# Kernel tuning notes

Hardware: AMD Instinct MI355X
Metric: run time of the kernel (lower is better)

## Reference

```python
import jax, jax.numpy as jnp
import numpy as np

B, S, D = 1, 2048, 4096
H, HKV, HD = 32, 8, 128
MAX_SEQ = 4096
EPS = 1e-5


def rmsnorm(x, w, eps=EPS):
    var = jnp.mean(x * x, axis=-1, keepdims=True)
    return w * (x * jax.lax.rsqrt(var + eps))


def rotate_half_interleaved(x):
    x1 = x[..., ::2]
    x2 = x[..., 1::2]
    return jnp.stack((-x2, x1), axis=-1).reshape(x.shape)


def setup_inputs() -> dict:
    key = jax.random.key(0)
    ks = jax.random.split(key, 8)
    hidden_states = jax.random.normal(ks[0], (B, S, D), dtype=jnp.float32)
    # realistic interleaved RoPE tables: each frequency repeated twice along head_dim
    inv_freq = 1.0 / (10000.0 ** (np.arange(0, HD, 2, dtype=np.float32) / HD))
    pos = np.arange(S, dtype=np.float32)
    ang = pos[:, None] * inv_freq[None, :]            # [S, HD/2]
    ang = np.repeat(ang, 2, axis=-1)                   # [S, HD] interleaved
    cos = jnp.asarray(np.cos(ang))[None].repeat(B, axis=0)  # [B, S, HD]
    sin = jnp.asarray(np.sin(ang))[None].repeat(B, axis=0)
    scale = 1.0 / np.sqrt(D)
    return {
        "hidden_states": hidden_states,
        "cos": cos,
        "sin": sin,
        "k_cache": jnp.zeros((B, MAX_SEQ, HKV, HD), dtype=jnp.float32),
        "v_cache": jnp.zeros((B, MAX_SEQ, HKV, HD), dtype=jnp.float32),
        "Wq": jax.random.normal(ks[1], (D, H * HD), dtype=jnp.float32) * scale,
        "Wk": jax.random.normal(ks[2], (D, HKV * HD), dtype=jnp.float32) * scale,
        "Wv": jax.random.normal(ks[3], (D, HKV * HD), dtype=jnp.float32) * scale,
        "Wo": jax.random.normal(ks[4], (H * HD, D), dtype=jnp.float32) * scale,
        "rms_weight": jnp.ones((D,), dtype=jnp.float32),
        "position_ids": jnp.arange(S, dtype=jnp.int64 if jax.config.jax_enable_x64 else jnp.int32),
        "seq_len": S,
    }


def reference(hidden_states, cos, sin, k_cache, v_cache, Wq, Wk, Wv, Wo,
              rms_weight, position_ids, seq_len):
    residual = hidden_states
    h = rmsnorm(hidden_states, rms_weight)
    b, s = h.shape[:2]

    q = jnp.einsum('bsd,de->bse', h, Wq).reshape(b, s, H, HD)
    k = jnp.einsum('bsd,de->bse', h, Wk).reshape(b, s, HKV, HD)
    v = jnp.einsum('bsd,de->bse', h, Wv).reshape(b, s, HKV, HD)

    # interleaved RoPE, cos/sin broadcast over head axis (unsqueeze_dim=-2)
    c = cos[:, :, None, :]
    si = sin[:, :, None, :]
    q = q * c + rotate_half_interleaved(q) * si
    k = k * c + rotate_half_interleaved(k) * si

    # KV-cache scatter at position_ids (repeat_factor == 1 here)
    k_cache_new = k_cache.at[:, position_ids].set(k)
    v_cache_new = v_cache.at[:, position_ids].set(v)

    # prefill path (new_tok_seq_len > 1): causal SDPA with GQA over fresh K/V
    group = H // HKV
    k_full = jnp.repeat(k, group, axis=2)  # [b, s, H, HD]
    v_full = jnp.repeat(v, group, axis=2)
    qh = q.transpose(0, 2, 1, 3)           # bhqd
    kh = k_full.transpose(0, 2, 1, 3)
    vh = v_full.transpose(0, 2, 1, 3)
    scores = jnp.einsum('bhqd,bhkd->bhqk', qh, kh) / jnp.sqrt(jnp.float32(HD))
    causal = jnp.tril(jnp.ones((s, s), dtype=bool))
    scores = jnp.where(causal[None, None], scores, jnp.finfo(scores.dtype).min)
    probs = jax.nn.softmax(scores, axis=-1)
    attn = jnp.einsum('bhqk,bhkd->bhqd', probs, vh)
    attn = attn.transpose(0, 2, 1, 3).reshape(b, s, H * HD)

    out = jnp.einsum('bse,ed->bsd', attn, Wo)
    with_residual = residual + out
    return with_residual, k_cache_new, v_cache_new
```

## Files before the change

kernel.cpp:

```cpp
#include <hip/hip_runtime.h>
#include <hip/hip_bf16.h>
#include <cstdint>

#define S_LEN 2048
#define DMODEL 4096
#define NHEAD 32
#define NKV 8
#define HDIM 128
#define MAXSEQ 4096
#define NQKV 6144

typedef __bf16 bf16x8 __attribute__((ext_vector_type(8)));
typedef float f32x4 __attribute__((ext_vector_type(4)));
typedef short s16x4 __attribute__((ext_vector_type(4)));

__device__ __forceinline__ short f2bf(float f) {
  unsigned u = __builtin_bit_cast(unsigned, f);
  u += 0x7fffu + ((u >> 16) & 1u);
  return (short)(u >> 16);
}

__device__ __forceinline__ void gload_lds16(const void* g, const void* l) {
  __builtin_amdgcn_global_load_lds((const __attribute__((address_space(1))) unsigned*)g,
                                   (__attribute__((address_space(3))) unsigned*)(l), 16, 0, 0);
}

template<int N> __device__ __forceinline__ void vwait() {
  if constexpr (N == 0) asm volatile("s_waitcnt vmcnt(0)" ::: "memory");
  else if constexpr (N == 1) asm volatile("s_waitcnt vmcnt(1)" ::: "memory");
  else if constexpr (N == 2) asm volatile("s_waitcnt vmcnt(2)" ::: "memory");
  else if constexpr (N == 3) asm volatile("s_waitcnt vmcnt(3)" ::: "memory");
  else if constexpr (N == 4) asm volatile("s_waitcnt vmcnt(4)" ::: "memory");
}

__global__ __launch_bounds__(256) void rmsnorm_kernel(const float* __restrict__ x,
                                                      const float* __restrict__ w,
                                                      short* __restrict__ out) {
  const int row = blockIdx.x, tid = threadIdx.x;
  const float4* xr = (const float4*)(x + (size_t)row * DMODEL);
  const float4* wr = (const float4*)w;
  float4 v[4];
  float ss = 0.f;
#pragma unroll
  for (int i = 0; i < 4; ++i) {
    v[i] = xr[tid + i * 256];
    ss += v[i].x * v[i].x + v[i].y * v[i].y + v[i].z * v[i].z + v[i].w * v[i].w;
  }
#pragma unroll
  for (int m = 32; m; m >>= 1) ss += __shfl_down(ss, m, 64);
  __shared__ float red[4];
  if ((tid & 63) == 0) red[tid >> 6] = ss;
  __syncthreads();
  float tot = red[0] + red[1] + red[2] + red[3];
  float sc = rsqrtf(tot * (1.f / DMODEL) + 1e-5f);
#pragma unroll
  for (int i = 0; i < 4; ++i) {
    float4 wv = wr[tid + i * 256];
    s16x4 o;
    o[0] = f2bf(v[i].x * sc * wv.x);
    o[1] = f2bf(v[i].y * sc * wv.y);
    o[2] = f2bf(v[i].z * sc * wv.z);
    o[3] = f2bf(v[i].w * sc * wv.w);
    *(s16x4*)&out[(size_t)row * DMODEL + (size_t)(tid + i * 256) * 4] = o;
  }
}

__global__ __launch_bounds__(256) void cast_transpose_all(const float* __restrict__ Wq,
                                                          const float* __restrict__ Wk,
                                                          const float* __restrict__ Wv,
                                                          const float* __restrict__ Wo,
                                                          short* __restrict__ WqkvT,
                                                          short* __restrict__ WoT) {
  const int z = blockIdx.z;
  const float* src;
  short* dst;
  int cols;
  if (z == 0)      { src = Wq; dst = WqkvT;                            cols = 4096; }
  else if (z == 1) { src = Wk; dst = WqkvT + (size_t)4096 * 4096;      cols = 1024; }
  else if (z == 2) { src = Wv; dst = WqkvT + (size_t)5120 * 4096;      cols = 1024; }
  else             { src = Wo; dst = WoT;                              cols = 4096; }
  const int c0 = blockIdx.x * 32, r0 = blockIdx.y * 32;
  if (c0 >= cols) return;
  __shared__ float tile[32][33];
  const int tx = threadIdx.x, ty = threadIdx.y;
#pragma unroll
  for (int i = ty; i < 32; i += 8) tile[i][tx] = src[(size_t)(r0 + i) * cols + c0 + tx];
  __syncthreads();
  const int tid = ty * 32 + tx;
#pragma unroll
  for (int rep = 0; rep < 2; ++rep) {
    int w = rep * 256 + tid;
    int i = w >> 4, pr = (w & 15) * 2;
    short2 o;
    o.x = f2bf(tile[pr][i]);
    o.y = f2bf(tile[pr + 1][i]);
    *(short2*)&dst[(size_t)(c0 + i) * 4096 + r0 + pr] = o;
  }
}

__global__ __launch_bounds__(256) void v_transpose(const float* __restrict__ QKV,
                                                   float* __restrict__ vc,
                                                   short* __restrict__ vt) {
  __shared__ float tile[32][33];
  const int d0 = blockIdx.x * 32, s0 = blockIdx.y * 32, g = blockIdx.z;
  const int tx = threadIdx.x, ty = threadIdx.y;
#pragma unroll
  for (int i = ty; i < 32; i += 8) {
    float v = QKV[(size_t)(s0 + i) * NQKV + (NHEAD + NKV) * HDIM + g * HDIM + d0 + tx];
    tile[i][tx] = v;
    vc[(size_t)(s0 + i) * (NKV * HDIM) + g * HDIM + d0 + tx] = v;
  }
  __syncthreads();
  const int tid = ty * 32 + tx;
#pragma unroll
  for (int rep = 0; rep < 2; ++rep) {
    int w = rep * 256 + tid;
    int i = w >> 4, pr = (w & 15) * 2;
    short2 o;
    o.x = f2bf(tile[pr][i]);
    o.y = f2bf(tile[pr + 1][i]);
    *(short2*)&vt[((size_t)g * HDIM + d0 + i) * S_LEN + s0 + pr] = o;
  }
}


template<int NF, int KS, int MH>
__device__ __forceinline__ void ph_load(const short* __restrict__ AsH, const short* __restrict__ BsB,
                                        const int lrow, const int quad, const int wn,
                                        bf16x8 (&aR)[4], bf16x8 (&bR)[2][NF]) {
  const int xr = lrow & 7;
#pragma unroll
  for (int f = 0; f < 4; ++f)
    aR[f] = *(const bf16x8*)&AsH[((((MH * 4 + f) * 16 + lrow) * 8) + ((KS * 4 + quad) ^ xr)) * 8];
  if constexpr (MH == 0) {
#pragma unroll
    for (int f = 0; f < NF; ++f) {
      int rB = wn * (16 * NF) + f * 16 + lrow;
      bR[KS][f] = *(const bf16x8*)&BsB[((rB * 8) + ((KS * 4 + quad) ^ xr)) * 8];
    }
  }
}

template<int NF, int KS, int MH>
__device__ __forceinline__ void ph_mfma(bf16x8 (&aR)[4], bf16x8 (&bR)[2][NF], f32x4 (&acc)[8][NF]) {
#pragma unroll
  for (int f = 0; f < 4; ++f)
#pragma unroll
    for (int n = 0; n < NF; ++n)
      acc[MH * 4 + f][n] =
          __builtin_amdgcn_mfma_f32_16x16x32_bf16(aR[f], bR[KS][n], acc[MH * 4 + f][n], 0, 0, 0);
}

template<int NF>
__global__ __launch_bounds__(512, 2) void gemm256(const short* __restrict__ A,
                                                  const short* __restrict__ Bt,
                                                  float* __restrict__ C,
                                                  const float* __restrict__ resid,
                                                  int M, int N, int K) {
  extern __shared__ __align__(16) short smem[];
  short* As = smem;
  short* Bs = smem + 32768;
  const int tid = threadIdx.x;
  const int lane = tid & 63, wave = tid >> 6;
  const int wm = wave >> 2, wn = wave & 3;
  const int lrow = lane & 15, quad = lane >> 4;
  const int m0 = blockIdx.y * 256, n0 = blockIdx.x * (64 * NF);
  const int srow = tid >> 3;
  const int scol = ((tid & 7) ^ (srow & 7)) << 3;
  const short* Ag = A + (size_t)m0 * K;
  const short* Bg = Bt + (size_t)n0 * K;
  const int nk = K >> 6;
  constexpr int G1 = NF - (NF >> 1);
  constexpr int G2 = NF >> 1;

#define STAGE_A(b, h, kt) do { \
    const short* g_ = Ag + (size_t)((h) * 128 + srow) * K + (size_t)(kt) * 64 + scol; \
    short* l_ = As + ((b) * 2 + (h)) * 8192 + wave * 512; \
    gload_lds16(g_, l_); \
    gload_lds16(g_ + (size_t)64 * K, l_ + 4096); \
  } while (0)
#define STAGE_BG(b, gr, kt) do { \
    const short* g_ = Bg + (size_t)((gr) * 64 + srow) * K + (size_t)(kt) * 64 + scol; \
    short* l_ = Bs + (b) * (NF * 4096) + (gr) * 4096 + wave * 512; \
    gload_lds16(g_, l_); \
  } while (0)
#define VW_COND if (more) { vwait<NF>(); } else { vwait<0>(); }
#define PHASE(BUF, KS, MH, STMT, VW) \
  ph_load<NF, KS, MH>(As + ((BUF) * 2 + wm) * 8192, Bs + (BUF) * (NF * 4096), \
                      lrow, quad, wn, aR, bR); \
  STMT; \
  VW \
  __builtin_amdgcn_s_barrier(); \
  asm volatile("s_waitcnt lgkmcnt(0)" ::: "memory"); \
  __builtin_amdgcn_s_setprio(1); \
  ph_mfma<NF, KS, MH>(aR, bR, acc); \
  __builtin_amdgcn_s_setprio(0); \
  __builtin_amdgcn_s_barrier();

  f32x4 acc[8][NF] = {};
  bf16x8 aR[4], bR[2][NF];

  STAGE_A(0, 0, 0); STAGE_A(0, 1, 0);
#pragma unroll
  for (int g = 0; g < NF; ++g) STAGE_BG(0, g, 0);
#pragma unroll
  for (int g = 0; g < NF; ++g) STAGE_BG(1, g, 1);
  vwait<NF>();
  __builtin_amdgcn_s_barrier();

  const int niter = nk >> 1;
  for (int i = 0; i < niter; ++i) {
    const int t = 2 * i;
    const bool more = (t + 2 < nk);
    PHASE(0, 0, 0, STAGE_A(1, 0, t + 1), )
    PHASE(0, 0, 1, STAGE_A(1, 1, t + 1), )
    PHASE(0, 1, 0,
          if (more) { _Pragma("unroll") for (int g = 0; g < G1; ++g) STAGE_BG(0, g, t + 2); }, )
    PHASE(0, 1, 1,
          if (more) { _Pragma("unroll") for (int g = G1; g < NF; ++g) STAGE_BG(0, g, t + 2); },
          VW_COND)
    PHASE(1, 0, 0, if (more) { STAGE_A(0, 0, t + 2); }, )
    PHASE(1, 0, 1, if (more) { STAGE_A(0, 1, t + 2); }, )
    PHASE(1, 1, 0,
          if (more) { _Pragma("unroll") for (int g = 0; g < G1; ++g) STAGE_BG(1, g, t + 3); }, )
    PHASE(1, 1, 1,
          if (more) { _Pragma("unroll") for (int g = G1; g < NF; ++g) STAGE_BG(1, g, t + 3); },
          vwait<NF>();)
  }

#pragma unroll
  for (int fm = 0; fm < 8; ++fm)
#pragma unroll
    for (int fn = 0; fn < NF; ++fn) {
      int row = m0 + wm * 128 + fm * 16 + quad * 4;
      int col = n0 + wn * (16 * NF) + fn * 16 + lrow;
#pragma unroll
      for (int r = 0; r < 4; ++r) {
        float v = acc[fm][fn][r];
        size_t o = (size_t)(row + r) * N + col;
        if (resid) v += resid[o];
        C[o] = v;
      }
    }
#undef STAGE_A
#undef STAGE_BG
#undef VW_COND
#undef PHASE
}

__global__ __launch_bounds__(256) void rope_kernel(const float* __restrict__ QKV,
                                                   const float* __restrict__ cosb,
                                                   const float* __restrict__ sinb,
                                                   short* __restrict__ qo,
                                                   short* __restrict__ ko,
                                                   float* __restrict__ kc,
                                                   float* __restrict__ vc) {
  const int s = blockIdx.x, tid = threadIdx.x;
  const float4* r4 = (const float4*)(QKV + (size_t)s * NQKV);
  const float qscale = 0.08838834764831845f;
#pragma unroll
  for (int it = 0; it < 5; ++it) {
    int i = it * 256 + tid;
    float4 x = r4[i];
    int e = i * 4;
    int d = e & 127;
    float4 c = *(const float4*)&cosb[(size_t)s * HDIM + d];
    float4 si = *(const float4*)&sinb[(size_t)s * HDIM + d];
    float o0 = x.x * c.x - x.y * si.x;
    float o1 = x.y * c.y + x.x * si.y;
    float o2 = x.z * c.z - x.w * si.z;
    float o3 = x.w * c.w + x.z * si.w;
    if (e < NHEAD * HDIM) {
      int hh = e >> 7;
      s16x4 ov;
      ov[0] = f2bf(o0 * qscale); ov[1] = f2bf(o1 * qscale);
      ov[2] = f2bf(o2 * qscale); ov[3] = f2bf(o3 * qscale);
      *(s16x4*)&qo[((size_t)hh * S_LEN + s) * HDIM + d] = ov;
    } else {
      int ek = e - NHEAD * HDIM;
      int g = ek >> 7;
      s16x4 ov;
      ov[0] = f2bf(o0); ov[1] = f2bf(o1); ov[2] = f2bf(o2); ov[3] = f2bf(o3);
      *(s16x4*)&ko[((size_t)g * S_LEN + s) * HDIM + d] = ov;
      *(float4*)&kc[(size_t)s * (NKV * HDIM) + ek] = make_float4(o0, o1, o2, o3);
    }
  }
  {
    const size_t base = (size_t)S_LEN * NKV * HDIM;
    const size_t i = (size_t)s * 256 + tid;
    const float4 z = make_float4(0.f, 0.f, 0.f, 0.f);
    ((float4*)(kc + base))[i] = z;
    ((float4*)(vc + base))[i] = z;
  }
}

#define TKEY 128
__global__ __launch_bounds__(256, 1) void attn_kernel(const short* __restrict__ Q,
                                                      const short* __restrict__ Kb,
                                                      const short* __restrict__ Vt,
                                                      short* __restrict__ out) {
  extern __shared__ __align__(16) short smem[];
  short* Ks = smem;
  short* Vs = smem + 32768;
  short* Ps = smem + 65536;
  const int tid = threadIdx.x;
  const int lane = tid & 63, wave = tid >> 6;
  const int lrow = lane & 15, quad = lane >> 4;
  const int g = blockIdx.x & 7, p = blockIdx.x >> 3;
  const int h = g * 4 + wave;
  const float L2E = 1.44269504f;
  const short* Kg = Kb + (size_t)g * S_LEN * HDIM;
  const short* Vg = Vt + (size_t)g * HDIM * S_LEN;
  short* Pw = Ps + wave * 1024;

#pragma unroll 1
  for (int ph = 0; ph < 2; ++ph) {
    const int qt = ph ? (63 - p) : p;
    const int nt = (qt >> 2) + 1;

    bf16x8 qf[2][4];
#pragma unroll
    for (int i = 0; i < 2; ++i)
#pragma unroll
      for (int kf = 0; kf < 4; ++kf)
        qf[i][kf] = *(const bf16x8*)&Q[((size_t)h * S_LEN + qt * 32 + i * 16 + lrow) * HDIM + kf * 32 + quad * 8];

    f32x4 O[2][8] = {};
    float mrun[2][4], lrun[2][4];
#pragma unroll
    for (int i = 0; i < 2; ++i)
#pragma unroll
      for (int r = 0; r < 4; ++r) { mrun[i][r] = -1e30f; lrun[i][r] = 0.f; }

#pragma unroll
    for (int ii = 0; ii < 8; ++ii) {
      int s = (wave * 8 + ii) * 64 + lane;
      int r = s >> 4, gg = (s & 15) ^ (r & 15);
      gload_lds16(Kg + (size_t)r * HDIM + gg * 8, Ks + (wave * 8 + ii) * 512);
    }
#pragma unroll
    for (int ii = 0; ii < 8; ++ii) {
      int s = (wave * 8 + ii) * 64 + lane;
      int d = s >> 4, kg = (s & 15) ^ (d & 15);
      gload_lds16(Vg + (size_t)d * S_LEN + kg * 8, Vs + (wave * 8 + ii) * 512);
    }
    __syncthreads();

#pragma unroll 1
    for (int t = 0; t < nt; ++t) {
      const int bsel = t & 1;
      if (t + 1 < nt) {
        const int kb2 = (t + 1) * TKEY, o = (1 - bsel) * 16384;
#pragma unroll
        for (int ii = 0; ii < 8; ++ii) {
          int s = (wave * 8 + ii) * 64 + lane;
          int r = s >> 4, gg = (s & 15) ^ (r & 15);
          gload_lds16(Kg + (size_t)(kb2 + r) * HDIM + gg * 8, Ks + o + (wave * 8 + ii) * 512);
        }
#pragma unroll
        for (int ii = 0; ii < 8; ++ii) {
          int s = (wave * 8 + ii) * 64 + lane;
          int d = s >> 4, kg = (s & 15) ^ (d & 15);
          gload_lds16(Vg + (size_t)d * S_LEN + kb2 + kg * 8, Vs + o + (wave * 8 + ii) * 512);
        }
      }
      const short* Kc = Ks + bsel * 16384;
      const short* Vc = Vs + bsel * 16384;

      f32x4 sc[2][8] = {};
#pragma unroll
      for (int c = 0; c < 8; ++c) {
        int r = c * 16 + lrow;
#pragma unroll
        for (int kf = 0; kf < 4; ++kf) {
          int slot = r * 16 + ((kf * 4 + quad) ^ lrow);
          bf16x8 kfr = *(const bf16x8*)&Kc[slot * 8];
          sc[0][c] = __builtin_amdgcn_mfma_f32_16x16x32_bf16(qf[0][kf], kfr, sc[0][c], 0, 0, 0);
          sc[1][c] = __builtin_amdgcn_mfma_f32_16x16x32_bf16(qf[1][kf], kfr, sc[1][c], 0, 0, 0);
        }
      }

      const int kb = t * TKEY;
      const bool last = (t == nt - 1);
#pragma unroll
      for (int i = 0; i < 2; ++i) {
        if (last) {
#pragma unroll
          for (int c = 0; c < 8; ++c) {
            int key = kb + c * 16 + lrow;
#pragma unroll
            for (int r = 0; r < 4; ++r) {
              int row = qt * 32 + i * 16 + quad * 4 + r;
              if (key > row) sc[i][c][r] = -1e30f;
            }
          }
        }
        float tm[4];
#pragma unroll
        for (int r = 0; r < 4; ++r) tm[r] = sc[i][0][r];
#pragma unroll
        for (int c = 1; c < 8; ++c)
#pragma unroll
          for (int r = 0; r < 4; ++r) tm[r] = fmaxf(tm[r], sc[i][c][r]);
#pragma unroll
        for (int msk = 1; msk <= 8; msk <<= 1)
#pragma unroll
          for (int r = 0; r < 4; ++r) tm[r] = fmaxf(tm[r], __shfl_xor(tm[r], msk, 64));
#pragma unroll
        for (int r = 0; r < 4; ++r) {
          float nm = fmaxf(mrun[i][r], tm[r]);
          float alpha = exp2f((mrun[i][r] - nm) * L2E);
          mrun[i][r] = nm;
          lrun[i][r] *= alpha;
#pragma unroll
          for (int jd = 0; jd < 8; ++jd) O[i][jd][r] *= alpha;
        }
        float rs[4] = {0.f, 0.f, 0.f, 0.f};
#pragma unroll
        for (int c = 0; c < 8; ++c)
#pragma unroll
          for (int r = 0; r < 4; ++r) {
            float pv = exp2f((sc[i][c][r] - mrun[i][r]) * L2E);
            sc[i][c][r] = pv;
            rs[r] += pv;
          }
#pragma unroll
        for (int msk = 1; msk <= 8; msk <<= 1)
#pragma unroll
          for (int r = 0; r < 4; ++r) rs[r] += __shfl_xor(rs[r], msk, 64);
#pragma unroll
        for (int r = 0; r < 4; ++r) lrun[i][r] += rs[r];
      }

#pragma unroll
      for (int ks = 0; ks < 4; ++ks) {
#pragma unroll
        for (int i = 0; i < 2; ++i)
#pragma unroll
          for (int cc = 0; cc < 2; ++cc) {
            int c = ks * 2 + cc;
            int kg = cc * 2 + (lrow >> 3), off = lrow & 7;
#pragma unroll
            for (int r = 0; r < 4; ++r) {
              int q2 = i * 16 + quad * 4 + r;
              int slot = q2 * 4 + (kg ^ (q2 & 3) ^ ((q2 >> 2) & 3));
              Pw[slot * 8 + off] = f2bf(sc[i][c][r]);
            }
          }
        bf16x8 pa[2];
#pragma unroll
        for (int i = 0; i < 2; ++i) {
          int q2 = i * 16 + lrow;
          int slot = q2 * 4 + (quad ^ (q2 & 3) ^ ((q2 >> 2) & 3));
          pa[i] = *(const bf16x8*)&Pw[slot * 8];
        }
#pragma unroll
        for (int jd = 0; jd < 8; ++jd) {
          int d = jd * 16 + lrow;
          int slotv = d * 16 + ((ks * 4 + quad) ^ lrow);
          bf16x8 vb = *(const bf16x8*)&Vc[slotv * 8];
          O[0][jd] = __builtin_amdgcn_mfma_f32_16x16x32_bf16(pa[0], vb, O[0][jd], 0, 0, 0);
          O[1][jd] = __builtin_amdgcn_mfma_f32_16x16x32_bf16(pa[1], vb, O[1][jd], 0, 0, 0);
        }
      }
      __syncthreads();
    }

#pragma unroll
    for (int i = 0; i < 2; ++i)
#pragma unroll
      for (int r = 0; r < 4; ++r) {
        float inv = 1.f / lrun[i][r];
        int row = qt * 32 + i * 16 + quad * 4 + r;
#pragma unroll
        for (int jd = 0; jd < 8; ++jd)
          out[(size_t)row * DMODEL + h * HDIM + jd * 16 + lrow] = f2bf(O[i][jd][r] * inv);
      }
    __syncthreads();
  }
}

extern "C" void kernel_launch(void* const* d_in, const int* in_sizes, int n_in,
                              void* d_out, int out_size, void* d_ws, size_t ws_size,
                              hipStream_t stream) {
  const float* hs   = (const float*)d_in[0];
  const float* cosb = (const float*)d_in[1];
  const float* sinb = (const float*)d_in[2];
  const float* Wq   = (const float*)d_in[5];
  const float* Wk   = (const float*)d_in[6];
  const float* Wv   = (const float*)d_in[7];
  const float* Wo   = (const float*)d_in[8];
  const float* rmsw = (const float*)d_in[9];

  float* outp = (float*)d_out;
  float* kc = outp + (size_t)S_LEN * DMODEL;
  float* vc = kc + (size_t)MAXSEQ * NKV * HDIM;

  char* p = (char*)d_ws;
  short* h_bf  = (short*)p; p += (size_t)S_LEN * DMODEL * 2;
  short* WqkvT = (short*)p; p += (size_t)NQKV * DMODEL * 2;
  short* WoT   = (short*)p; p += (size_t)DMODEL * DMODEL * 2;
  float* QKV   = (float*)p; p += (size_t)S_LEN * NQKV * 4;
  short* q_bf  = (short*)p; p += (size_t)NHEAD * S_LEN * HDIM * 2;
  short* k_bf  = (short*)p; p += (size_t)NKV * S_LEN * HDIM * 2;
  short* vt_bf = (short*)p; p += (size_t)NKV * HDIM * S_LEN * 2;
  short* attn_bf = h_bf;

  const int ATTN_LDS = 139264;
  hipFuncSetAttribute(reinterpret_cast<const void*>(attn_kernel),
                      hipFuncAttributeMaxDynamicSharedMemorySize, ATTN_LDS);
  const int GEMM_LDS3 = 65536 + 3 * 16384;
  const int GEMM_LDS2 = 65536 + 2 * 16384;
  hipFuncSetAttribute(reinterpret_cast<const void*>(gemm256<3>),
                      hipFuncAttributeMaxDynamicSharedMemorySize, GEMM_LDS3);
  hipFuncSetAttribute(reinterpret_cast<const void*>(gemm256<2>),
                      hipFuncAttributeMaxDynamicSharedMemorySize, GEMM_LDS2);

  rmsnorm_kernel<<<S_LEN, 256, 0, stream>>>(hs, rmsw, h_bf);
  cast_transpose_all<<<dim3(128, 128, 4), dim3(32, 8), 0, stream>>>(Wq, Wk, Wv, Wo, WqkvT, WoT);
  gemm256<3><<<dim3(NQKV / 192, S_LEN / 256), 512, GEMM_LDS3, stream>>>(h_bf, WqkvT, QKV, nullptr, S_LEN, NQKV, DMODEL);
  rope_kernel<<<S_LEN, 256, 0, stream>>>(QKV, cosb, sinb, q_bf, k_bf, kc, vc);
  v_transpose<<<dim3(HDIM / 32, S_LEN / 32, NKV), dim3(32, 8), 0, stream>>>(QKV, vc, vt_bf);
  attn_kernel<<<256, 256, ATTN_LDS, stream>>>(q_bf, k_bf, vt_bf, attn_bf);
  gemm256<2><<<dim3(DMODEL / 128, S_LEN / 256), 512, GEMM_LDS2, stream>>>(attn_bf, WoT, outp, hs, S_LEN, DMODEL, DMODEL);
}
```

Before: 586.7 us.

## Split attention work across 512 blocks with per-wave query tiles, single-buffer KV

The attention kernel changes its work split. Each block now covers two heads, and each wave pair handles a short and a long causal query tile at the same time, instead of processing two phases one after the other. The grid doubles to 512 blocks. K/V staging drops from double-buffered to a single buffer, which cuts LDS to about 72KB and allows two blocks per CU. The cost is that each K/V load is no longer overlapped with compute inside a block. Waves working on the short tile also sit idle through the barriers until the long tile finishes.

```diff
diff --git a/kernel.cpp b/kernel.cpp
--- a/kernel.cpp
+++ b/kernel.cpp
@@ -171,7 +171,6 @@
   const short* Bg = Bt + (size_t)n0 * K;
   const int nk = K >> 6;
   constexpr int G1 = NF - (NF >> 1);
-  constexpr int G2 = NF >> 1;
 
 #define STAGE_A(b, h, kt) do { \
     const short* g_ = Ag + (size_t)((h) * 128 + srow) * K + (size_t)(kt) * 64 + scol; \
@@ -295,78 +294,61 @@
 }
 
 #define TKEY 128
-__global__ __launch_bounds__(256, 1) void attn_kernel(const short* __restrict__ Q,
+__global__ __launch_bounds__(256, 2) void attn_kernel(const short* __restrict__ Q,
                                                       const short* __restrict__ Kb,
                                                       const short* __restrict__ Vt,
                                                       short* __restrict__ out) {
   extern __shared__ __align__(16) short smem[];
   short* Ks = smem;
-  short* Vs = smem + 32768;
-  short* Ps = smem + 65536;
+  short* Vs = smem + 16384;
+  short* Ps = smem + 32768;
   const int tid = threadIdx.x;
   const int lane = tid & 63, wave = tid >> 6;
   const int lrow = lane & 15, quad = lane >> 4;
-  const int g = blockIdx.x & 7, p = blockIdx.x >> 3;
-  const int h = g * 4 + wave;
+  const int g = blockIdx.x & 7;
+  const int rest = blockIdx.x >> 3;
+  const int hp = rest & 1, p = rest >> 1;
+  const int h = g * 4 + hp * 2 + (wave >> 1);
+  const int qt = (wave & 1) ? (63 - p) : p;
+  const int ntw = (qt >> 2) + 1;
+  const int ntmax = ((63 - p) >> 2) + 1;
   const float L2E = 1.44269504f;
   const short* Kg = Kb + (size_t)g * S_LEN * HDIM;
   const short* Vg = Vt + (size_t)g * HDIM * S_LEN;
   short* Pw = Ps + wave * 1024;
 
+  bf16x8 qf[2][4];
+#pragma unroll
+  for (int i = 0; i < 2; ++i)
+#pragma unroll
+    for (int kf = 0; kf < 4; ++kf)
+      qf[i][kf] = *(const bf16x8*)&Q[((size_t)h * S_LEN + qt * 32 + i * 16 + lrow) * HDIM + kf * 32 + quad * 8];
+
+  f32x4 O[2][8] = {};
+  float mrun[2][4], lrun[2][4];
+#pragma unroll
+  for (int i = 0; i < 2; ++i)
+#pragma unroll
+    for (int r = 0; r < 4; ++r) { mrun[i][r] = -1e30f; lrun[i][r] = 0.f; }
+
 #pragma unroll 1
-  for (int ph = 0; ph < 2; ++ph) {
-    const int qt = ph ? (63 - p) : p;
-    const int nt = (qt >> 2) + 1;
-
-    bf16x8 qf[2][4];
-#pragma unroll
-    for (int i = 0; i < 2; ++i)
-#pragma unroll
-      for (int kf = 0; kf < 4; ++kf)
-        qf[i][kf] = *(const bf16x8*)&Q[((size_t)h * S_LEN + qt * 32 + i * 16 + lrow) * HDIM + kf * 32 + quad * 8];
-
-    f32x4 O[2][8] = {};
-    float mrun[2][4], lrun[2][4];
-#pragma unroll
-    for (int i = 0; i < 2; ++i)
-#pragma unroll
-      for (int r = 0; r < 4; ++r) { mrun[i][r] = -1e30f; lrun[i][r] = 0.f; }
-
+  for (int t = 0; t < ntmax; ++t) {
+    const int kb = t * TKEY;
 #pragma unroll
     for (int ii = 0; ii < 8; ++ii) {
       int s = (wave * 8 + ii) * 64 + lane;
       int r = s >> 4, gg = (s & 15) ^ (r & 15);
-      gload_lds16(Kg + (size_t)r * HDIM + gg * 8, Ks + (wave * 8 + ii) * 512);
+      gload_lds16(Kg + (size_t)(kb + r) * HDIM + gg * 8, Ks + (wave * 8 + ii) * 512);
     }
 #pragma unroll
     for (int ii = 0; ii < 8; ++ii) {
       int s = (wave * 8 + ii) * 64 + lane;
       int d = s >> 4, kg = (s & 15) ^ (d & 15);
-      gload_lds16(Vg + (size_t)d * S_LEN + kg * 8, Vs + (wave * 8 + ii) * 512);
+      gload_lds16(Vg + (size_t)d * S_LEN + kb + kg * 8, Vs + (wave * 8 + ii) * 512);
     }
     __syncthreads();
 
-#pragma unroll 1
-    for (int t = 0; t < nt; ++t) {
-      const int bsel = t & 1;
-      if (t + 1 < nt) {
-        const int kb2 = (t + 1) * TKEY, o = (1 - bsel) * 16384;
-#pragma unroll
-        for (int ii = 0; ii < 8; ++ii) {
-          int s = (wave * 8 + ii) * 64 + lane;
-          int r = s >> 4, gg = (s & 15) ^ (r & 15);
-          gload_lds16(Kg + (size_t)(kb2 + r) * HDIM + gg * 8, Ks + o + (wave * 8 + ii) * 512);
-        }
-#pragma unroll
-        for (int ii = 0; ii < 8; ++ii) {
-          int s = (wave * 8 + ii) * 64 + lane;
-          int d = s >> 4, kg = (s & 15) ^ (d & 15);
-          gload_lds16(Vg + (size_t)d * S_LEN + kb2 + kg * 8, Vs + o + (wave * 8 + ii) * 512);
-        }
-      }
-      const short* Kc = Ks + bsel * 16384;
-      const short* Vc = Vs + bsel * 16384;
-
+    if (t < ntw) {
       f32x4 sc[2][8] = {};
 #pragma unroll
       for (int c = 0; c < 8; ++c) {
@@ -374,14 +356,13 @@
 #pragma unroll
         for (int kf = 0; kf < 4; ++kf) {
           int slot = r * 16 + ((kf * 4 + quad) ^ lrow);
-          bf16x8 kfr = *(const bf16x8*)&Kc[slot * 8];
+          bf16x8 kfr = *(const bf16x8*)&Ks[slot * 8];
           sc[0][c] = __builtin_amdgcn_mfma_f32_16x16x32_bf16(qf[0][kf], kfr, sc[0][c], 0, 0, 0);
           sc[1][c] = __builtin_amdgcn_mfma_f32_16x16x32_bf16(qf[1][kf], kfr, sc[1][c], 0, 0, 0);
         }
       }
 
-      const int kb = t * TKEY;
-      const bool last = (t == nt - 1);
+      const bool last = (t == ntw - 1);
 #pragma unroll
       for (int i = 0; i < 2; ++i) {
         if (last) {
@@ -458,26 +439,25 @@
         for (int jd = 0; jd < 8; ++jd) {
           int d = jd * 16 + lrow;
           int slotv = d * 16 + ((ks * 4 + quad) ^ lrow);
-          bf16x8 vb = *(const bf16x8*)&Vc[slotv * 8];
+          bf16x8 vb = *(const bf16x8*)&Vs[slotv * 8];
           O[0][jd] = __builtin_amdgcn_mfma_f32_16x16x32_bf16(pa[0], vb, O[0][jd], 0, 0, 0);
           O[1][jd] = __builtin_amdgcn_mfma_f32_16x16x32_bf16(pa[1], vb, O[1][jd], 0, 0, 0);
         }
       }
-      __syncthreads();
-    }
-
-#pragma unroll
-    for (int i = 0; i < 2; ++i)
-#pragma unroll
-      for (int r = 0; r < 4; ++r) {
-        float inv = 1.f / lrun[i][r];
-        int row = qt * 32 + i * 16 + quad * 4 + r;
-#pragma unroll
-        for (int jd = 0; jd < 8; ++jd)
-          out[(size_t)row * DMODEL + h * HDIM + jd * 16 + lrow] = f2bf(O[i][jd][r] * inv);
-      }
+    }
     __syncthreads();
   }
+
+#pragma unroll
+  for (int i = 0; i < 2; ++i)
+#pragma unroll
+    for (int r = 0; r < 4; ++r) {
+      float inv = 1.f / lrun[i][r];
+      int row = qt * 32 + i * 16 + quad * 4 + r;
+#pragma unroll
+      for (int jd = 0; jd < 8; ++jd)
+        out[(size_t)row * DMODEL + h * HDIM + jd * 16 + lrow] = f2bf(O[i][jd][r] * inv);
+    }
 }
 
 extern "C" void kernel_launch(void* const* d_in, const int* in_sizes, int n_in,
@@ -506,7 +486,7 @@
   short* vt_bf = (short*)p; p += (size_t)NKV * HDIM * S_LEN * 2;
   short* attn_bf = h_bf;
 
-  const int ATTN_LDS = 139264;
+  const int ATTN_LDS = 73728;
   hipFuncSetAttribute(reinterpret_cast<const void*>(attn_kernel),
                       hipFuncAttributeMaxDynamicSharedMemorySize, ATTN_LDS);
   const int GEMM_LDS3 = 65536 + 3 * 16384;
@@ -521,6 +501,6 @@
   gemm256<3><<<dim3(NQKV / 192, S_LEN / 256), 512, GEMM_LDS3, stream>>>(h_bf, WqkvT, QKV, nullptr, S_LEN, NQKV, DMODEL);
   rope_kernel<<<S_LEN, 256, 0, stream>>>(QKV, cosb, sinb, q_bf, k_bf, kc, vc);
   v_transpose<<<dim3(HDIM / 32, S_LEN / 32, NKV), dim3(32, 8), 0, stream>>>(QKV, vc, vt_bf);
-  attn_kernel<<<256, 256, ATTN_LDS, stream>>>(q_bf, k_bf, vt_bf, attn_bf);
+  attn_kernel<<<512, 256, ATTN_LDS, stream>>>(q_bf, k_bf, vt_bf, attn_bf);
   gemm256<2><<<dim3(DMODEL / 128, S_LEN / 256), 512, GEMM_LDS2, stream>>>(attn_bf, WoT, outp, hs, S_LEN, DMODEL, DMODEL);
 }
```

Result: slower. 702.9 us (+19.8%).
